# Optimization experiments

Hardware: AMD Instinct MI355X
Metric: run time of the kernel (lower is better)

The kernel has to match this reference:

```python
import jax, jax.numpy as jnp
import numpy as np

B, S, D, H, F, L = 16, 512, 512, 8, 2048, 3  # L layers: 1 in blocks_1 + 2 in blocks_2
DK = D // H
EPS = 1e-5

def setup_inputs():
    key = jax.random.key(0)
    ks = jax.random.split(key, 10)
    sc = 1.0 / np.sqrt(D)
    return dict(
        q_embed_data=jax.random.normal(ks[0], (B, S, D), jnp.float32),
        qa_embed_data=jax.random.normal(ks[1], (B, S, D), jnp.float32),
        Wk=jax.random.normal(ks[2], (L, D, D), jnp.float32) * sc,
        bk=jnp.zeros((L, D), jnp.float32),
        Wv=jax.random.normal(ks[3], (L, D, D), jnp.float32) * sc,
        bv=jnp.zeros((L, D), jnp.float32),
        Wo=jax.random.normal(ks[4], (L, D, D), jnp.float32) * sc,
        bo=jnp.zeros((L, D), jnp.float32),
        gammas=jax.random.normal(ks[5], (L, H, 1, 1), jnp.float32) * 0.5,
        ln1_g=jnp.ones((L, D), jnp.float32),
        ln1_b=jnp.zeros((L, D), jnp.float32),
        W1=jax.random.normal(ks[6], (L, D, F), jnp.float32) * sc,
        b1=jnp.zeros((L, F), jnp.float32),
        W2=jax.random.normal(ks[7], (L, F, D), jnp.float32) * (1.0 / np.sqrt(F)),
        b2=jnp.zeros((L, D), jnp.float32),
        ln2_g=jnp.ones((L, D), jnp.float32),
        ln2_b=jnp.zeros((L, D), jnp.float32),
    )

def _ln(x, g, b):
    m = jnp.mean(x, -1, keepdims=True)
    v = jnp.mean((x - m) ** 2, -1, keepdims=True)
    return (x - m) * jax.lax.rsqrt(v + EPS) * g + b

def _attention(q, k, v, mask, gamma):
    # q,k,v: [B,H,S,DK]; mask: [1,1,S,S] bool; gamma: [H,1,1]
    scores = jnp.einsum('bhid,bhjd->bhij', q, k) / np.sqrt(DK)
    maskf = mask.astype(scores.dtype)
    # first (no-grad in torch) softmax pass for distance decay
    p = jax.nn.softmax(jnp.where(mask, scores, -1e32), axis=-1) * maskf
    distcum = jnp.cumsum(p, axis=-1)
    disttot = jnp.sum(p, axis=-1, keepdims=True)
    idx = jnp.arange(scores.shape[-1])
    pos = jnp.abs(idx[None, :] - idx[:, None]).astype(scores.dtype)[None, None]
    dist = jax.lax.stop_gradient(
        jnp.sqrt(jnp.clip((disttot - distcum) * pos, 0.0, None)))
    g = -jax.nn.softplus(gamma)[None]  # [1,H,1,1]
    total_effect = jnp.clip(jnp.exp(dist * g), 1e-5, 1e5)
    scores = jnp.where(mask, scores * total_effect, -1e32)
    attn = jax.nn.softmax(scores, axis=-1)
    return jnp.einsum('bhij,bhjd->bhid', attn, v)

def _mha(q_in, k_in, v_in, mask, Wk, bk, Wv, bv, Wo, bo, gamma):
    bsz = q_in.shape[0]
    def proj(x, W, b):
        return (x @ W + b).reshape(bsz, -1, H, DK).transpose(0, 2, 1, 3)
    q = proj(q_in, Wk, bk)  # kq_same=True -> q uses k_linear
    k = proj(k_in, Wk, bk)
    v = proj(v_in, Wv, bv)
    o = _attention(q, k, v, mask, gamma)
    o = o.transpose(0, 2, 1, 3).reshape(bsz, -1, D)
    return o @ Wo + bo

def _block(i, mask, query, key, values, apply_pos, P):
    q2 = _mha(query, key, values, mask, P['Wk'][i], P['bk'][i], P['Wv'][i],
              P['bv'][i], P['Wo'][i], P['bo'][i], P['gammas'][i])
    x = _ln(query + q2, P['ln1_g'][i], P['ln1_b'][i])
    if apply_pos:
        h = jax.nn.relu(x @ P['W1'][i] + P['b1'][i]) @ P['W2'][i] + P['b2'][i]
        x = _ln(x + h, P['ln2_g'][i], P['ln2_b'][i])
    return x

def reference(q_embed_data, qa_embed_data, Wk, bk, Wv, bv, Wo, bo, gammas,
              ln1_g, ln1_b, W1, b1, W2, b2, ln2_g, ln2_b):
    P = dict(Wk=Wk, bk=bk, Wv=Wv, bv=bv, Wo=Wo, bo=bo, gammas=gammas,
             ln1_g=ln1_g, ln1_b=ln1_b, W1=W1, b1=b1, W2=W2, b2=b2,
             ln2_g=ln2_g, ln2_b=ln2_b)
    s = q_embed_data.shape[1]
    mask1 = jnp.tril(jnp.ones((s, s), bool))[None, None]        # mask==1: current+past
    mask0 = jnp.tril(jnp.ones((s, s), bool), -1)[None, None]    # mask==0: strictly past
    y = qa_embed_data
    x = q_embed_data
    y = _block(0, mask1, y, y, y, True, P)    # blocks_1: knowledge encoder
    x = _block(1, mask1, x, x, x, False, P)   # blocks_2: question encoder (no FFN)
    x = _block(2, mask0, x, x, y, True, P)    # blocks_2: knowledge retriever
    return x
```

## Files before the change

kernel.cpp:

```cpp
#include <hip/hip_runtime.h>
#include <hip/hip_bf16.h>

#define Bdim 16
#define Sdim 512
#define Ddim 512
#define Hdim 8
#define DKdim 64
#define Fdim 2048
#define Mrows (Bdim * Sdim)

typedef __attribute__((ext_vector_type(8))) short  frag16;
typedef __attribute__((ext_vector_type(4))) float  f32x4;
typedef __attribute__((ext_vector_type(8))) unsigned short ushort8;
typedef __attribute__((ext_vector_type(4))) unsigned short ushort4v;

#if defined(__has_builtin)
#  if __has_builtin(__builtin_amdgcn_exp2f)
#    define EXP2(x) __builtin_amdgcn_exp2f(x)
#  endif
#endif
#ifndef EXP2
#  define EXP2(x) __expf((x) * 0.6931471805599453f)
#endif
#define SC2 0.18033688011112042f

__device__ __forceinline__ unsigned short f2b(float x) {
    union { float f; unsigned int u; } v; v.f = x;
    unsigned int r = (v.u + 0x7FFFu + ((v.u >> 16) & 1u)) >> 16;
    return (unsigned short)r;
}

__global__ __launch_bounds__(256) void gemm_mfma(
    const __hip_bfloat16* __restrict__ A, const __hip_bfloat16* __restrict__ Bt,
    const float* __restrict__ bias, const float* __restrict__ R,
    float* __restrict__ Cf, unsigned short* __restrict__ Cb,
    int M, int N, int K, int do_relu)
{
    __shared__ short As[2][128 * 32];
    __shared__ short Bs[2][128 * 32];

    const int t = threadIdx.x;
    const int lane = t & 63;
    const int wave = t >> 6;

    const int gx = gridDim.x;
    const int nb = gx * gridDim.y;
    const int lid = blockIdx.x + gx * blockIdx.y;
    const int wid = (lid & 7) * (nb >> 3) + (lid >> 3);
    const int bm = (wid / gx) * 128;
    const int bn = (wid % gx) * 128;

    const int wm = (wave >> 1) * 64;
    const int wn = (wave & 1) * 64;

    f32x4 acc[4][4] = {};
    const int lrow = lane >> 2;
    const int lcol = (lane & 3) * 8;

    auto stage = [&](int k0, int buf) {
#pragma unroll
        for (int i = 0; i < 2; ++i) {
            const int chunk = wave * 2 + i;
            const int row = chunk * 16 + lrow;
            const __hip_bfloat16* ga = A + (size_t)(bm + row) * K + k0 + lcol;
            const __hip_bfloat16* gb = Bt + (size_t)(bn + row) * K + k0 + lcol;
            __builtin_amdgcn_global_load_lds(
                (const __attribute__((address_space(1))) unsigned int*)ga,
                (__attribute__((address_space(3))) unsigned int*)(&As[buf][chunk * 512]),
                16, 0, 0);
            __builtin_amdgcn_global_load_lds(
                (const __attribute__((address_space(1))) unsigned int*)gb,
                (__attribute__((address_space(3))) unsigned int*)(&Bs[buf][chunk * 512]),
                16, 0, 0);
        }
    };

    const int fr = lane & 15;
    const int quad = lane >> 4;
    const int nk = K >> 5;

    stage(0, 0);
    __syncthreads();

    for (int it = 0; it < nk; ++it) {
        const int buf = it & 1;
        if (it + 1 < nk) stage((it + 1) << 5, buf ^ 1);
        frag16 af[4], bfr[4];
#pragma unroll
        for (int i = 0; i < 4; ++i) {
            af[i]  = *(const frag16*)(&As[buf][(wm + i * 16 + fr) * 32 + quad * 8]);
            bfr[i] = *(const frag16*)(&Bs[buf][(wn + i * 16 + fr) * 32 + quad * 8]);
        }
#pragma unroll
        for (int mi = 0; mi < 4; ++mi)
#pragma unroll
            for (int ni = 0; ni < 4; ++ni)
                acc[mi][ni] = __builtin_amdgcn_mfma_f32_16x16x32_bf16(
                    af[mi], bfr[ni], acc[mi][ni], 0, 0, 0);
        __syncthreads();
    }

#pragma unroll
    for (int mi = 0; mi < 4; ++mi) {
#pragma unroll
        for (int r = 0; r < 4; ++r) {
            const int m = bm + wm + mi * 16 + quad * 4 + r;
#pragma unroll
            for (int ni = 0; ni < 4; ++ni) {
                const int n = bn + wn + ni * 16 + fr;
                float v = acc[mi][ni][r] + bias[n];
                if (R) v += R[(size_t)m * N + n];
                if (do_relu) v = fmaxf(v, 0.f);
                if (Cf) Cf[(size_t)m * N + n] = v;
                if (Cb) Cb[(size_t)m * N + n] = f2b(v);
            }
        }
    }
}

__global__ __launch_bounds__(256) void gemm_n64(
    const unsigned short* __restrict__ A0, const unsigned short* __restrict__ A1,
    const unsigned short* __restrict__ B0, const unsigned short* __restrict__ B1,
    const float* __restrict__ bias0, const float* __restrict__ bias1,
    const float* __restrict__ R, float* __restrict__ Cf,
    unsigned short* __restrict__ Cb, unsigned short* __restrict__ CbT,
    int K)
{
    const int NN = 512;
    __shared__ short As[2][128 * 64];
    __shared__ short Bs[2][64 * 64];

    const int trans = blockIdx.z;
    const unsigned short* A  = trans ? A1 : A0;
    const unsigned short* Bt = trans ? B1 : B0;
    const float* bias        = trans ? bias1 : bias0;

    const int t = threadIdx.x;
    const int lane = t & 63;
    const int wave = t >> 6;

    const int lid = blockIdx.x + 8 * blockIdx.y;
    const int wid = (lid & 7) * 64 + (lid >> 3);
    const int bm = (wid >> 3) * 128;
    const int bn = (wid & 7) * 64;

    const int wm = (wave >> 1) * 64;
    const int wn = (wave & 1) * 32;

    f32x4 acc[4][2] = {};

    const int srcslot = (((lane & 7) ^ (lane >> 3)) << 3);
    const int rsub = lane >> 3;

    auto stage = [&](int k0, int buf) {
#pragma unroll
        for (int i = 0; i < 4; ++i) {
            const int row = i * 32 + wave * 8 + rsub;
            const unsigned short* ga = A + (size_t)(bm + row) * K + k0 + srcslot;
            __builtin_amdgcn_global_load_lds(
                (const __attribute__((address_space(1))) unsigned int*)ga,
                (__attribute__((address_space(3))) unsigned int*)(&As[buf][(i * 256 + wave * 64) * 8]),
                16, 0, 0);
        }
#pragma unroll
        for (int i = 0; i < 2; ++i) {
            const int row = i * 32 + wave * 8 + rsub;
            const unsigned short* gb = Bt + (size_t)(bn + row) * K + k0 + srcslot;
            __builtin_amdgcn_global_load_lds(
                (const __attribute__((address_space(1))) unsigned int*)gb,
                (__attribute__((address_space(3))) unsigned int*)(&Bs[buf][(i * 256 + wave * 64) * 8]),
                16, 0, 0);
        }
    };

    const int fr = lane & 15;
    const int quad = lane >> 4;
    const int sw = (fr & 7) << 3;
    const int nk = K >> 6;

    stage(0, 0);
    __syncthreads();

    for (int it = 0; it < nk; ++it) {
        const int buf = it & 1;
        if (it + 1 < nk) stage((it + 1) << 6, buf ^ 1);
        frag16 af[2][4], bfr[2][2];
#pragma unroll
        for (int ks = 0; ks < 2; ++ks) {
            const int col = (ks * 32 + quad * 8) ^ sw;
#pragma unroll
            for (int i = 0; i < 4; ++i)
                af[ks][i] = *(const frag16*)(&As[buf][(wm + i * 16 + fr) * 64 + col]);
#pragma unroll
            for (int i = 0; i < 2; ++i)
                bfr[ks][i] = *(const frag16*)(&Bs[buf][(wn + i * 16 + fr) * 64 + col]);
        }
#pragma unroll
        for (int ks = 0; ks < 2; ++ks)
#pragma unroll
            for (int mi = 0; mi < 4; ++mi)
#pragma unroll
                for (int ni = 0; ni < 2; ++ni)
                    acc[mi][ni] = __builtin_amdgcn_mfma_f32_16x16x32_bf16(
                        af[ks][mi], bfr[ks][ni], acc[mi][ni], 0, 0, 0);
        __syncthreads();
    }

    if (trans) {
#pragma unroll
        for (int mi = 0; mi < 4; ++mi)
#pragma unroll
            for (int ni = 0; ni < 2; ++ni) {
                const int m = bm + wm + mi * 16 + quad * 4;
                const int n = bn + wn + ni * 16 + fr;
                ushort4v o;
#pragma unroll
                for (int r = 0; r < 4; ++r) o[r] = f2b(acc[mi][ni][r] + bias[n]);
                const int bb = m >> 9, s = m & 511;
                const int hh = n >> 6, dd = n & 63;
                *(ushort4v*)(CbT + (((size_t)((bb * Hdim + hh) * DKdim + dd)) << 9) + s) = o;
            }
        return;
    }

#pragma unroll
    for (int mi = 0; mi < 4; ++mi) {
#pragma unroll
        for (int r = 0; r < 4; ++r) {
            const int m = bm + wm + mi * 16 + quad * 4 + r;
#pragma unroll
            for (int ni = 0; ni < 2; ++ni) {
                const int n = bn + wn + ni * 16 + fr;
                float v = acc[mi][ni][r] + bias[n];
                if (R) v += R[(size_t)m * NN + n];
                if (Cf) Cf[(size_t)m * NN + n] = v;
                if (Cb) Cb[(size_t)m * NN + n] = f2b(v);
            }
        }
    }
}

__global__ __launch_bounds__(256) void gemm_kv4(
    const unsigned short* __restrict__ Ya, const unsigned short* __restrict__ Xa,
    const unsigned short* __restrict__ BtK0, const unsigned short* __restrict__ BtV0,
    const unsigned short* __restrict__ BtK1, const unsigned short* __restrict__ BtV1,
    const float* __restrict__ bk0, const float* __restrict__ bv0,
    const float* __restrict__ bk1, const float* __restrict__ bv1,
    unsigned short* __restrict__ K0, unsigned short* __restrict__ V0t,
    unsigned short* __restrict__ K1, unsigned short* __restrict__ V1t)
{
    const int K = 512;
    __shared__ short As[2][128 * 64];
    __shared__ short Bs[2][64 * 64];

    const int z = blockIdx.z;
    const unsigned short* A  = (z < 2) ? Ya : Xa;
    const unsigned short* Bt = (z == 0) ? BtK0 : (z == 1) ? BtV0 : (z == 2) ? BtK1 : BtV1;
    const float* bias        = (z == 0) ? bk0 : (z == 1) ? bv0 : (z == 2) ? bk1 : bv1;
    const int trans = z & 1;

    const int t = threadIdx.x;
    const int lane = t & 63;
    const int wave = t >> 6;

    const int lid = blockIdx.x + 8 * blockIdx.y;
    const int wid = (lid & 7) * 64 + (lid >> 3);
    const int bm = (wid >> 3) * 128;
    const int bn = (wid & 7) * 64;

    const int wm = (wave >> 1) * 64;
    const int wn = (wave & 1) * 32;

    f32x4 acc[4][2] = {};
    const int srcslot = (((lane & 7) ^ (lane >> 3)) << 3);
    const int rsub = lane >> 3;

    auto stage = [&](int k0, int buf) {
#pragma unroll
        for (int i = 0; i < 4; ++i) {
            const int row = i * 32 + wave * 8 + rsub;
            const unsigned short* ga = A + (size_t)(bm + row) * K + k0 + srcslot;
            __builtin_amdgcn_global_load_lds(
                (const __attribute__((address_space(1))) unsigned int*)ga,
                (__attribute__((address_space(3))) unsigned int*)(&As[buf][(i * 256 + wave * 64) * 8]),
                16, 0, 0);
        }
#pragma unroll
        for (int i = 0; i < 2; ++i) {
            const int row = i * 32 + wave * 8 + rsub;
            const unsigned short* gb = Bt + (size_t)(bn + row) * K + k0 + srcslot;
            __builtin_amdgcn_global_load_lds(
                (const __attribute__((address_space(1))) unsigned int*)gb,
                (__attribute__((address_space(3))) unsigned int*)(&Bs[buf][(i * 256 + wave * 64) * 8]),
                16, 0, 0);
        }
    };

    const int fr = lane & 15;
    const int quad = lane >> 4;
    const int sw = (fr & 7) << 3;
    const int nk = K >> 6;

    stage(0, 0);
    __syncthreads();

    for (int it = 0; it < nk; ++it) {
        const int buf = it & 1;
        if (it + 1 < nk) stage((it + 1) << 6, buf ^ 1);
        frag16 af[2][4], bfr[2][2];
#pragma unroll
        for (int ks = 0; ks < 2; ++ks) {
            const int col = (ks * 32 + quad * 8) ^ sw;
#pragma unroll
            for (int i = 0; i < 4; ++i)
                af[ks][i] = *(const frag16*)(&As[buf][(wm + i * 16 + fr) * 64 + col]);
#pragma unroll
            for (int i = 0; i < 2; ++i)
                bfr[ks][i] = *(const frag16*)(&Bs[buf][(wn + i * 16 + fr) * 64 + col]);
        }
#pragma unroll
        for (int ks = 0; ks < 2; ++ks)
#pragma unroll
            for (int mi = 0; mi < 4; ++mi)
#pragma unroll
                for (int ni = 0; ni < 2; ++ni)
                    acc[mi][ni] = __builtin_amdgcn_mfma_f32_16x16x32_bf16(
                        af[ks][mi], bfr[ks][ni], acc[mi][ni], 0, 0, 0);
        __syncthreads();
    }

    if (trans) {
        unsigned short* CbT = (z == 1) ? V0t : V1t;
#pragma unroll
        for (int mi = 0; mi < 4; ++mi)
#pragma unroll
            for (int ni = 0; ni < 2; ++ni) {
                const int m = bm + wm + mi * 16 + quad * 4;
                const int n = bn + wn + ni * 16 + fr;
                ushort4v o;
#pragma unroll
                for (int r = 0; r < 4; ++r) o[r] = f2b(acc[mi][ni][r] + bias[n]);
                const int bb = m >> 9, s = m & 511;
                const int hh = n >> 6, dd = n & 63;
                *(ushort4v*)(CbT + (((size_t)((bb * Hdim + hh) * DKdim + dd)) << 9) + s) = o;
            }
    } else {
        unsigned short* Cb = (z == 0) ? K0 : K1;
#pragma unroll
        for (int mi = 0; mi < 4; ++mi)
#pragma unroll
            for (int r = 0; r < 4; ++r) {
                const int m = bm + wm + mi * 16 + quad * 4 + r;
#pragma unroll
                for (int ni = 0; ni < 2; ++ni) {
                    const int n = bn + wn + ni * 16 + fr;
                    Cb[(size_t)m * 512 + n] = f2b(acc[mi][ni][r] + bias[n]);
                }
            }
    }
}

__global__ __launch_bounds__(256) void gemm_o2(
    const unsigned short* __restrict__ A0, const unsigned short* __restrict__ A1,
    const unsigned short* __restrict__ B0, const unsigned short* __restrict__ B1,
    const float* __restrict__ bias0, const float* __restrict__ bias1,
    const float* __restrict__ R0, const float* __restrict__ R1,
    float* __restrict__ C0, float* __restrict__ C1)
{
    const int K = 512;
    __shared__ short As[2][128 * 64];
    __shared__ short Bs[2][64 * 64];

    const int z = blockIdx.z;
    const unsigned short* A  = z ? A1 : A0;
    const unsigned short* Bt = z ? B1 : B0;
    const float* bias        = z ? bias1 : bias0;
    const float* R           = z ? R1 : R0;
    float* Cf                = z ? C1 : C0;

    const int t = threadIdx.x;
    const int lane = t & 63;
    const int wave = t >> 6;

    const int lid = blockIdx.x + 8 * blockIdx.y;
    const int wid = (lid & 7) * 64 + (lid >> 3);
    const int bm = (wid >> 3) * 128;
    const int bn = (wid & 7) * 64;

    const int wm = (wave >> 1) * 64;
    const int wn = (wave & 1) * 32;

    f32x4 acc[4][2] = {};
    const int srcslot = (((lane & 7) ^ (lane >> 3)) << 3);
    const int rsub = lane >> 3;

    auto stage = [&](int k0, int buf) {
#pragma unroll
        for (int i = 0; i < 4; ++i) {
            const int row = i * 32 + wave * 8 + rsub;
            const unsigned short* ga = A + (size_t)(bm + row) * K + k0 + srcslot;
            __builtin_amdgcn_global_load_lds(
                (const __attribute__((address_space(1))) unsigned int*)ga,
                (__attribute__((address_space(3))) unsigned int*)(&As[buf][(i * 256 + wave * 64) * 8]),
                16, 0, 0);
        }
#pragma unroll
        for (int i = 0; i < 2; ++i) {
            const int row = i * 32 + wave * 8 + rsub;
            const unsigned short* gb = Bt + (size_t)(bn + row) * K + k0 + srcslot;
            __builtin_amdgcn_global_load_lds(
                (const __attribute__((address_space(1))) unsigned int*)gb,
                (__attribute__((address_space(3))) unsigned int*)(&Bs[buf][(i * 256 + wave * 64) * 8]),
                16, 0, 0);
        }
    };

    const int fr = lane & 15;
    const int quad = lane >> 4;
    const int sw = (fr & 7) << 3;
    const int nk = K >> 6;

    stage(0, 0);
    __syncthreads();

    for (int it = 0; it < nk; ++it) {
        const int buf = it & 1;
        if (it + 1 < nk) stage((it + 1) << 6, buf ^ 1);
        frag16 af[2][4], bfr[2][2];
#pragma unroll
        for (int ks = 0; ks < 2; ++ks) {
            const int col = (ks * 32 + quad * 8) ^ sw;
#pragma unroll
            for (int i = 0; i < 4; ++i)
                af[ks][i] = *(const frag16*)(&As[buf][(wm + i * 16 + fr) * 64 + col]);
#pragma unroll
            for (int i = 0; i < 2; ++i)
                bfr[ks][i] = *(const frag16*)(&Bs[buf][(wn + i * 16 + fr) * 64 + col]);
        }
#pragma unroll
        for (int ks = 0; ks < 2; ++ks)
#pragma unroll
            for (int mi = 0; mi < 4; ++mi)
#pragma unroll
                for (int ni = 0; ni < 2; ++ni)
                    acc[mi][ni] = __builtin_amdgcn_mfma_f32_16x16x32_bf16(
                        af[ks][mi], bfr[ks][ni], acc[mi][ni], 0, 0, 0);
        __syncthreads();
    }

#pragma unroll
    for (int mi = 0; mi < 4; ++mi) {
#pragma unroll
        for (int r = 0; r < 4; ++r) {
            const int m = bm + wm + mi * 16 + quad * 4 + r;
#pragma unroll
            for (int ni = 0; ni < 2; ++ni) {
                const int n = bn + wn + ni * 16 + fr;
                Cf[(size_t)m * 512 + n] = acc[mi][ni][r] + bias[n] + R[(size_t)m * 512 + n];
            }
        }
    }
}

__global__ __launch_bounds__(256) void conv_b2(
    const float* __restrict__ X0, unsigned short* __restrict__ Y0,
    const float* __restrict__ X1, unsigned short* __restrict__ Y1,
    int halfBlocks)
{
    const int bid = blockIdx.x;
    const float* X = (bid < halfBlocks) ? X0 : X1;
    unsigned short* Y = (bid < halfBlocks) ? Y0 : Y1;
    const int lb = (bid < halfBlocks) ? bid : bid - halfBlocks;
    const size_t i = ((size_t)lb * 256 + threadIdx.x) * 8;
    float4 a = *(const float4*)(X + i);
    float4 b = *(const float4*)(X + i + 4);
    ushort8 o;
    o[0] = f2b(a.x); o[1] = f2b(a.y); o[2] = f2b(a.z); o[3] = f2b(a.w);
    o[4] = f2b(b.x); o[5] = f2b(b.y); o[6] = f2b(b.z); o[7] = f2b(b.w);
    *(ushort8*)(Y + i) = o;
}

__global__ __launch_bounds__(256) void wtrans_all(
    const float* __restrict__ Wk, const float* __restrict__ Wv,
    const float* __restrict__ Wo, const float* __restrict__ W1,
    const float* __restrict__ W2, unsigned short* __restrict__ dst)
{
    const int bid = blockIdx.x;
    const float* src; unsigned short* d; int K, N, tk, tn;
    if (bid < 576) {
        const int mat = bid >> 6, tile = bid & 63;
        const int l = mat / 3, wch = mat % 3;
        const float* W = (wch == 0) ? Wk : (wch == 1) ? Wv : Wo;
        src = W + (size_t)l * 262144;
        d = dst + (size_t)mat * 262144;
        K = 512; N = 512; tn = tile & 7; tk = tile >> 3;
    } else if (bid < 1088) {
        const int idx = bid - 576, l2 = idx >> 8, tile = idx & 255;
        src = W1 + (size_t)(l2 * 2) * (512 * 2048);
        d = dst + 9 * 262144 + (size_t)l2 * (512 * 2048);
        K = 512; N = 2048; tn = tile & 31; tk = tile >> 5;
    } else {
        const int idx = bid - 1088, l2 = idx >> 8, tile = idx & 255;
        src = W2 + (size_t)(l2 * 2) * (2048 * 512);
        d = dst + 9 * 262144 + 2 * (512 * 2048) + (size_t)l2 * (2048 * 512);
        K = 2048; N = 512; tn = tile & 7; tk = tile >> 3;
    }
    const int n0 = tn * 64, k0 = tk * 64;
    __shared__ float T[64][65];
    const int t = threadIdx.x;
    const int kl = t >> 4, n4 = (t & 15) << 2;
#pragma unroll
    for (int it = 0; it < 4; ++it) {
        const int k = kl + it * 16;
        float4 v = *(const float4*)(src + (size_t)(k0 + k) * N + n0 + n4);
        T[n4 + 0][k] = v.x; T[n4 + 1][k] = v.y;
        T[n4 + 2][k] = v.z; T[n4 + 3][k] = v.w;
    }
    __syncthreads();
    const int nl = t >> 3, k8 = (t & 7) << 3;
#pragma unroll
    for (int it = 0; it < 2; ++it) {
        const int n = nl + it * 32;
        ushort8 o;
#pragma unroll
        for (int c = 0; c < 8; ++c) o[c] = f2b(T[n][k8 + c]);
        *(ushort8*)(d + (size_t)(n0 + n) * K + k0 + k8) = o;
    }
}

__global__ __launch_bounds__(256, 8) void attn_flash8(
    const unsigned short* __restrict__ Kb0, const unsigned short* __restrict__ Vt0,
    const unsigned short* __restrict__ Kb1, const unsigned short* __restrict__ Vt1,
    const float* __restrict__ gam,
    unsigned short* __restrict__ Ob0, unsigned short* __restrict__ Ob1,
    int mask_type, int dual)
{
    __shared__ float CTw[16 * 33];
    __shared__ unsigned short Pst[4][16 * 36];
    __shared__ float S1s[4][16];
    __shared__ float S2s[4][16];
    __shared__ float OaccA[16 * 66];
    __shared__ float OaccB[16 * 66];

    int bh, layer;
    if (dual) { layer = blockIdx.x & 1; bh = blockIdx.x >> 1; }
    else      { layer = 0;              bh = blockIdx.x; }
    const unsigned short* Kb = layer ? Kb1 : Kb0;
    const unsigned short* Vt = layer ? Vt1 : Vt0;
    unsigned short* Ob       = layer ? Ob1 : Ob0;
    const float* g           = gam + layer * Hdim;

    const int h = bh & 7, b = bh >> 3;
    const int rk = blockIdx.y;
    const int tile = mask_type ? (31 - rk) : (rk == 0 ? 0 : 32 - rk);

    const int t = threadIdx.x, lane = t & 63, w = t >> 6;
    const int quad = lane >> 4, fr = lane & 15;
    const int q0 = tile * 16;
    const int iRow = q0 + fr;

    const unsigned short* kbase = Kb + (size_t)b * Sdim * Ddim + h * DKdim;
    const unsigned short* vtb = Vt + (size_t)(b * Hdim + h) * DKdim * Sdim;
    const float gneg2 = -log1pf(__expf(g[h])) * 1.4426950408889634f;

    frag16 aq0 = *(const frag16*)(kbase + (size_t)(q0 + fr) * Ddim + quad * 8);
    frag16 aq1 = *(const frag16*)(kbase + (size_t)(q0 + fr) * Ddim + 32 + quad * 8);

    float psum = 0.f;
    for (int jn = w; jn <= tile; jn += 4) {
        frag16 k0 = *(const frag16*)(kbase + (size_t)(jn * 16 + fr) * Ddim + quad * 8);
        frag16 k1 = *(const frag16*)(kbase + (size_t)(jn * 16 + fr) * Ddim + 32 + quad * 8);
        f32x4 z = {0.f, 0.f, 0.f, 0.f};
        z = __builtin_amdgcn_mfma_f32_16x16x32_bf16(k0, aq0, z, 0, 0, 0);
        z = __builtin_amdgcn_mfma_f32_16x16x32_bf16(k1, aq1, z, 0, 0, 0);
        float tq = 0.f;
        if (jn < tile) {
#pragma unroll
            for (int r = 0; r < 4; ++r) tq += EXP2(z[r] * SC2);
        } else {
#pragma unroll
            for (int r = 0; r < 4; ++r) {
                const bool valid = mask_type ? (quad * 4 + r <= fr)
                                             : (quad * 4 + r < fr);
                tq += valid ? EXP2(z[r] * SC2) : 0.f;
            }
        }
        psum += tq;
        float tt = tq;
        tt += __shfl_xor(tt, 16);
        tt += __shfl_xor(tt, 32);
        if (quad == 0) CTw[fr * 33 + jn] = tt;
    }
    {
        float s1 = psum;
        s1 += __shfl_xor(s1, 16);
        s1 += __shfl_xor(s1, 32);
        if (lane < 16) S1s[w][lane] = s1;
    }
    __syncthreads();

    if (w == 0 && lane < 16) {
        float run = 0.f;
        for (int jn = tile; jn >= 0; --jn) {
            const float tv = CTw[lane * 33 + jn];
            CTw[lane * 33 + jn] = run;
            run += tv;
        }
    }
    __syncthreads();

    const float rsum1 = 1.f / (S1s[0][fr] + S1s[1][fr] + S1s[2][fr] + S1s[3][fr]);
    unsigned short* Pw = Pst[w];
    const bool fm_blk = (mask_type == 0) && (tile == 0);
    const bool fmrow = fm_blk && (fr == 0);
    const int umax = fm_blk ? (Sdim / 32 - 1) : (tile >> 1);
    float sum2p = 0.f;
    f32x4 oacc[4] = {};

    for (int u = umax - w; u >= 0; u -= 4) {
#pragma unroll
        for (int half = 0; half < 2; ++half) {
            const int jn = 2 * u + half;
            uint2 pku;
            if (jn > tile) {
                const unsigned int pv = fmrow ? 0x3F803F80u : 0u;
                pku.x = pv; pku.y = pv;
                sum2p += fmrow ? 4.f : 0.f;
            } else {
                frag16 k0 = *(const frag16*)(kbase + (size_t)(jn * 16 + fr) * Ddim + quad * 8);
                frag16 k1 = *(const frag16*)(kbase + (size_t)(jn * 16 + fr) * Ddim + 32 + quad * 8);
                f32x4 z = {0.f, 0.f, 0.f, 0.f};
                z = __builtin_amdgcn_mfma_f32_16x16x32_bf16(k0, aq0, z, 0, 0, 0);
                z = __builtin_amdgcn_mfma_f32_16x16x32_bf16(k1, aq1, z, 0, 0, 0);
                const bool full = (jn < tile);
                float s2r[4], lsuf[4];
                float tq = 0.f;
#pragma unroll
                for (int r = 3; r >= 0; --r) {
                    lsuf[r] = tq;
                    s2r[r] = z[r] * SC2;
                    float e1 = EXP2(s2r[r]);
                    if (!full) {
                        const bool valid = mask_type ? (quad * 4 + r <= fr)
                                                     : (quad * 4 + r < fr);
                        e1 = valid ? e1 : 0.f;
                    }
                    tq += e1;
                }
                float incl = tq;
                {
                    float u1 = __shfl_down(incl, 16);
                    incl += (quad < 3) ? u1 : 0.f;
                    float u2 = __shfl_down(incl, 32);
                    incl += (quad < 2) ? u2 : 0.f;
                }
                const float base = CTw[fr * 33 + jn] + (incl - tq);
                const float pos0 = (float)(iRow - (jn * 16 + quad * 4));
                float e2v[4];
#pragma unroll
                for (int r = 0; r < 4; ++r) {
                    const float ratio = (base + lsuf[r]) * rsum1;
                    const float arg = ratio * fabsf(pos0 - (float)r);
                    const float te = fmaxf(EXP2(gneg2 * sqrtf(arg)), 1e-5f);
                    float e2 = EXP2(s2r[r] * te);
                    if (!full) {
                        const bool valid = mask_type ? (quad * 4 + r <= fr)
                                                     : (quad * 4 + r < fr);
                        e2 = valid ? e2 : (fmrow ? 1.f : 0.f);
                    }
                    sum2p += e2;
                    e2v[r] = e2;
                }
                union { __hip_bfloat162 hh; unsigned int u; } c0, c1;
                c0.hh = __float22bfloat162_rn(make_float2(e2v[0], e2v[1]));
                c1.hh = __float22bfloat162_rn(make_float2(e2v[2], e2v[3]));
                pku.x = c0.u; pku.y = c1.u;
            }
            *(uint2*)(Pw + fr * 36 + half * 16 + quad * 4) = pku;
        }
        frag16 pf = *(const frag16*)(Pw + fr * 36 + quad * 8);
        const int jb = u * 32;
#pragma unroll
        for (int dt = 0; dt < 4; ++dt) {
            frag16 vf = *(const frag16*)(vtb + (size_t)(dt * 16 + fr) * Sdim + jb + quad * 8);
            oacc[dt] = __builtin_amdgcn_mfma_f32_16x16x32_bf16(pf, vf, oacc[dt], 0, 0, 0);
        }
    }

    {
        float s2 = sum2p;
        s2 += __shfl_xor(s2, 16);
        s2 += __shfl_xor(s2, 32);
        if (lane < 16) S2s[w][lane] = s2;
    }
    if (w == 1) {
#pragma unroll
        for (int dt = 0; dt < 4; ++dt)
#pragma unroll
            for (int r = 0; r < 4; ++r)
                OaccA[(quad * 4 + r) * 66 + dt * 16 + fr] = oacc[dt][r];
    }
    if (w == 3) {
#pragma unroll
        for (int dt = 0; dt < 4; ++dt)
#pragma unroll
            for (int r = 0; r < 4; ++r)
                OaccB[(quad * 4 + r) * 66 + dt * 16 + fr] = oacc[dt][r];
    }
    __syncthreads();
    if (w == 0) {
#pragma unroll
        for (int dt = 0; dt < 4; ++dt)
#pragma unroll
            for (int r = 0; r < 4; ++r)
                oacc[dt][r] += OaccA[(quad * 4 + r) * 66 + dt * 16 + fr];
    }
    if (w == 2) {
#pragma unroll
        for (int dt = 0; dt < 4; ++dt)
#pragma unroll
            for (int r = 0; r < 4; ++r)
                oacc[dt][r] += OaccB[(quad * 4 + r) * 66 + dt * 16 + fr];
    }
    __syncthreads();
    if (w == 2) {
#pragma unroll
        for (int dt = 0; dt < 4; ++dt)
#pragma unroll
            for (int r = 0; r < 4; ++r)
                OaccA[(quad * 4 + r) * 66 + dt * 16 + fr] = oacc[dt][r];
    }
    __syncthreads();

    if (w == 0) {
        const float rs2 = 1.f / (S2s[0][fr] + S2s[1][fr] + S2s[2][fr] + S2s[3][fr]);
        float rs2q[4];
#pragma unroll
        for (int r = 0; r < 4; ++r) rs2q[r] = __shfl(rs2, quad * 4 + r);

        unsigned short* obase = Ob + ((size_t)(b * Sdim + q0)) * Ddim + h * DKdim;
#pragma unroll
        for (int dt = 0; dt < 4; ++dt)
#pragma unroll
            for (int r = 0; r < 4; ++r) {
                const float v = oacc[dt][r] + OaccA[(quad * 4 + r) * 66 + dt * 16 + fr];
                obase[(size_t)(quad * 4 + r) * Ddim + dt * 16 + fr] = f2b(v * rs2q[r]);
            }
    }
}

__device__ __forceinline__ void ln_row(
    const float* __restrict__ X, const float* __restrict__ g,
    const float* __restrict__ bta, float* __restrict__ Y,
    unsigned short* __restrict__ Yb, int row, int t,
    float* r1, float* r2)
{
    const float* x = X + (size_t)row * Ddim;
    float a = x[t], b = x[t + 256];
    r1[t] = a + b;
    r2[t] = a * a + b * b;
    __syncthreads();
    for (int off = 128; off; off >>= 1) {
        if (t < off) { r1[t] += r1[t + off]; r2[t] += r2[t + off]; }
        __syncthreads();
    }
    float mean = r1[0] * (1.f / Ddim);
    float var = r2[0] * (1.f / Ddim) - mean * mean;
    float rs = rsqrtf(var + 1e-5f);
    float y0 = (a - mean) * rs * g[t] + bta[t];
    float y1 = (b - mean) * rs * g[t + 256] + bta[t + 256];
    if (Y) {
        float* y = Y + (size_t)row * Ddim;
        y[t] = y0;
        y[t + 256] = y1;
    }
    if (Yb) {
        unsigned short* yb = Yb + (size_t)row * Ddim;
        yb[t] = f2b(y0);
        yb[t + 256] = f2b(y1);
    }
}

__global__ __launch_bounds__(256) void ln_kernel(
    const float* __restrict__ X, const float* __restrict__ g,
    const float* __restrict__ bta, float* __restrict__ Y,
    unsigned short* __restrict__ Yb)
{
    __shared__ float r1[256], r2[256];
    ln_row(X, g, bta, Y, Yb, blockIdx.x, threadIdx.x, r1, r2);
}

__global__ __launch_bounds__(256) void ln_kernel2(
    const float* __restrict__ Xa, const float* __restrict__ ga,
    const float* __restrict__ ba, float* __restrict__ Ya,
    unsigned short* __restrict__ Yba,
    const float* __restrict__ Xb, const float* __restrict__ gb,
    const float* __restrict__ bb, float* __restrict__ Yb2,
    unsigned short* __restrict__ Ybb)
{
    __shared__ float r1[256], r2[256];
    const int row = blockIdx.x;
    if (row < Mrows)
        ln_row(Xa, ga, ba, Ya, Yba, row, threadIdx.x, r1, r2);
    else
        ln_row(Xb, gb, bb, Yb2, Ybb, row - Mrows, threadIdx.x, r1, r2);
}

extern "C" void kernel_launch(void* const* d_in, const int* in_sizes, int n_in,
                              void* d_out, int out_size, void* d_ws, size_t ws_size,
                              hipStream_t stream)
{
    const float* x0     = (const float*)d_in[0];
    const float* y0     = (const float*)d_in[1];
    const float* Wk     = (const float*)d_in[2];
    const float* bk     = (const float*)d_in[3];
    const float* Wv     = (const float*)d_in[4];
    const float* bv     = (const float*)d_in[5];
    const float* Wo     = (const float*)d_in[6];
    const float* bo     = (const float*)d_in[7];
    const float* gammas = (const float*)d_in[8];
    const float* ln1g   = (const float*)d_in[9];
    const float* ln1b   = (const float*)d_in[10];
    const float* W1     = (const float*)d_in[11];
    const float* b1     = (const float*)d_in[12];
    const float* W2     = (const float*)d_in[13];
    const float* b2     = (const float*)d_in[14];
    const float* ln2g   = (const float*)d_in[15];
    const float* ln2b   = (const float*)d_in[16];

    const size_t NBSD = (size_t)Mrows * Ddim;
    float* ws = (float*)d_ws;
    float* T1   = ws;
    float* X1   = T1 + NBSD;
    float* Xbuf = X1 + NBSD;
    unsigned short* Kbf = (unsigned short*)(Xbuf + NBSD);
    unsigned short* Vt  = Kbf + NBSD;
    unsigned short* AOb = Vt + NBSD;
    unsigned short* Abf = AOb + NBSD;
    unsigned short* Xbf = Abf + NBSD;
    unsigned short* Ybf = Xbf + NBSD;
    unsigned short* Hbb = Ybf + NBSD;
    unsigned short* WtAll = Hbb + (size_t)Mrows * Fdim;

    unsigned short* Xb_in = Hbb;
    unsigned short* AOb1  = Hbb + NBSD;
    unsigned short* Yb_in = Hbb + 2 * NBSD;
    unsigned short* Kbf1  = Abf;
    unsigned short* Vt1   = Ybf;
    float* T1b = (float*)d_out;

    auto WtK = [&](int l) { return WtAll + (size_t)(l * 3 + 0) * 262144; };
    auto WtV = [&](int l) { return WtAll + (size_t)(l * 3 + 1) * 262144; };
    auto WtO = [&](int l) { return WtAll + (size_t)(l * 3 + 2) * 262144; };
    auto Wt1 = [&](int l) { return WtAll + 9 * 262144 + (size_t)(l >> 1) * (512 * 2048); };
    auto Wt2 = [&](int l) { return WtAll + 9 * 262144 + 2 * (512 * 2048) + (size_t)(l >> 1) * (2048 * 512); };

    const int convBlocks = (int)(NBSD / 2048);

    wtrans_all<<<1600, 256, 0, stream>>>(Wk, Wv, Wo, W1, W2, WtAll);
    conv_b2<<<2 * convBlocks, 256, 0, stream>>>(y0, Yb_in, x0, Xb_in, convBlocks);
    gemm_kv4<<<dim3(8, 64, 4), 256, 0, stream>>>(
        Yb_in, Xb_in, WtK(0), WtV(0), WtK(1), WtV(1),
        bk, bv, bk + Ddim, bv + Ddim,
        Kbf, Vt, Kbf1, Vt1);
    attn_flash8<<<dim3(2 * Bdim * Hdim, Sdim / 16, 1), 256, 0, stream>>>(
        Kbf, Vt, Kbf1, Vt1, gammas, AOb, AOb1, 1, 1);
    gemm_o2<<<dim3(8, 64, 2), 256, 0, stream>>>(
        AOb, AOb1, WtO(0), WtO(1), bo, bo + Ddim, y0, x0, T1, T1b);
    ln_kernel2<<<2 * Mrows, 256, 0, stream>>>(
        T1, ln1g, ln1b, X1, Abf,
        T1b, ln1g + Ddim, ln1b + Ddim, Xbuf, Xbf);
    gemm_mfma<<<dim3(Fdim / 128, Mrows / 128), 256, 0, stream>>>(
        (const __hip_bfloat16*)Abf, (const __hip_bfloat16*)Wt1(0),
        b1, nullptr, nullptr, Hbb, Mrows, Fdim, Ddim, 1);
    gemm_n64<<<dim3(8, 64, 1), 256, 0, stream>>>(
        Hbb, Hbb, Wt2(0), Wt2(0), b2, b2,
        X1, T1, nullptr, nullptr, Fdim);
    ln_kernel<<<Mrows, 256, 0, stream>>>(T1, ln2g, ln2b, nullptr, Ybf);

    const int l = 2;
    gemm_n64<<<dim3(8, 64, 2), 256, 0, stream>>>(
        Xbf, Ybf, WtK(l), WtV(l), bk + l * Ddim, bv + l * Ddim,
        nullptr, nullptr, Kbf, Vt, Ddim);
    attn_flash8<<<dim3(Bdim * Hdim, Sdim / 16, 1), 256, 0, stream>>>(
        Kbf, Vt, Kbf, Vt, gammas + (size_t)l * Hdim, AOb, AOb, 0, 0);
    gemm_n64<<<dim3(8, 64, 1), 256, 0, stream>>>(
        AOb, AOb, WtO(l), WtO(l), bo + l * Ddim, bo + l * Ddim,
        Xbuf, T1, nullptr, nullptr, Ddim);
    ln_kernel<<<Mrows, 256, 0, stream>>>(T1,
        ln1g + (size_t)l * Ddim, ln1b + (size_t)l * Ddim, X1, Abf);
    gemm_mfma<<<dim3(Fdim / 128, Mrows / 128), 256, 0, stream>>>(
        (const __hip_bfloat16*)Abf, (const __hip_bfloat16*)Wt1(l),
        b1 + (size_t)l * Fdim, nullptr, nullptr, Hbb, Mrows, Fdim, Ddim, 1);
    gemm_n64<<<dim3(8, 64, 1), 256, 0, stream>>>(
        Hbb, Hbb, Wt2(l), Wt2(l), b2 + (size_t)l * Ddim, b2 + (size_t)l * Ddim,
        X1, T1, nullptr, nullptr, Fdim);
    ln_kernel<<<Mrows, 256, 0, stream>>>(T1,
        ln2g + (size_t)l * Ddim, ln2b + (size_t)l * Ddim, (float*)d_out, nullptr);
}
```

Measured before the change: 575.3 us.

## Split-K the FFN down-projection and fold partial sums into wave-per-row LayerNorm

The FFN second GEMM (K=2048) becomes a two-way split-K kernel. One K-half writes bias plus residual plus its partial sum, and the other writes a raw partial into a float buffer that aliases the AOb/Abf scratch space. The following LayerNorm adds the two partials. LayerNorm is also rewritten to use one wave per row with float4 loads and shuffle reductions, replacing the 256-thread shared-memory tree with its many barriers. The aim is more blocks for the down-projection and cheaper normalisation, at the cost of extra partial-buffer traffic and a reliance on the scratch aliasing being safe.

```diff
diff --git a/kernel.cpp b/kernel.cpp
--- a/kernel.cpp
+++ b/kernel.cpp
@@ -235,6 +235,105 @@
                 if (R) v += R[(size_t)m * NN + n];
                 if (Cf) Cf[(size_t)m * NN + n] = v;
                 if (Cb) Cb[(size_t)m * NN + n] = f2b(v);
+            }
+        }
+    }
+}
+
+__global__ __launch_bounds__(256) void gemm_ffn2(
+    const unsigned short* __restrict__ A, const unsigned short* __restrict__ Bt,
+    const float* __restrict__ bias, const float* __restrict__ R,
+    float* __restrict__ C0, float* __restrict__ C1)
+{
+    const int K = 2048, KH = 1024;
+    __shared__ short As[2][128 * 64];
+    __shared__ short Bs[2][64 * 64];
+
+    const int z = blockIdx.z;
+    const int kbase = z * KH;
+
+    const int t = threadIdx.x;
+    const int lane = t & 63;
+    const int wave = t >> 6;
+
+    const int lid = blockIdx.x + 8 * blockIdx.y;
+    const int wid = (lid & 7) * 64 + (lid >> 3);
+    const int bm = (wid >> 3) * 128;
+    const int bn = (wid & 7) * 64;
+
+    const int wm = (wave >> 1) * 64;
+    const int wn = (wave & 1) * 32;
+
+    f32x4 acc[4][2] = {};
+    const int srcslot = (((lane & 7) ^ (lane >> 3)) << 3);
+    const int rsub = lane >> 3;
+
+    auto stage = [&](int k0, int buf) {
+#pragma unroll
+        for (int i = 0; i < 4; ++i) {
+            const int row = i * 32 + wave * 8 + rsub;
+            const unsigned short* ga = A + (size_t)(bm + row) * K + k0 + srcslot;
+            __builtin_amdgcn_global_load_lds(
+                (const __attribute__((address_space(1))) unsigned int*)ga,
+                (__attribute__((address_space(3))) unsigned int*)(&As[buf][(i * 256 + wave * 64) * 8]),
+                16, 0, 0);
+        }
+#pragma unroll
+        for (int i = 0; i < 2; ++i) {
+            const int row = i * 32 + wave * 8 + rsub;
+            const unsigned short* gb = Bt + (size_t)(bn + row) * K + k0 + srcslot;
+            __builtin_amdgcn_global_load_lds(
+                (const __attribute__((address_space(1))) unsigned int*)gb,
+                (__attribute__((address_space(3))) unsigned int*)(&Bs[buf][(i * 256 + wave * 64) * 8]),
+                16, 0, 0);
+        }
+    };
+
+    const int fr = lane & 15;
+    const int quad = lane >> 4;
+    const int sw = (fr & 7) << 3;
+    const int nk = KH >> 6;
+
+    stage(kbase, 0);
+    __syncthreads();
+
+    for (int it = 0; it < nk; ++it) {
+        const int buf = it & 1;
+        if (it + 1 < nk) stage(kbase + ((it + 1) << 6), buf ^ 1);
+        frag16 af[2][4], bfr[2][2];
+#pragma unroll
+        for (int ks = 0; ks < 2; ++ks) {
+            const int col = (ks * 32 + quad * 8) ^ sw;
+#pragma unroll
+            for (int i = 0; i < 4; ++i)
+                af[ks][i] = *(const frag16*)(&As[buf][(wm + i * 16 + fr) * 64 + col]);
+#pragma unroll
+            for (int i = 0; i < 2; ++i)
+                bfr[ks][i] = *(const frag16*)(&Bs[buf][(wn + i * 16 + fr) * 64 + col]);
+        }
+#pragma unroll
+        for (int ks = 0; ks < 2; ++ks)
+#pragma unroll
+            for (int mi = 0; mi < 4; ++mi)
+#pragma unroll
+                for (int ni = 0; ni < 2; ++ni)
+                    acc[mi][ni] = __builtin_amdgcn_mfma_f32_16x16x32_bf16(
+                        af[ks][mi], bfr[ks][ni], acc[mi][ni], 0, 0, 0);
+        __syncthreads();
+    }
+
+#pragma unroll
+    for (int mi = 0; mi < 4; ++mi) {
+#pragma unroll
+        for (int r = 0; r < 4; ++r) {
+            const int m = bm + wm + mi * 16 + quad * 4 + r;
+#pragma unroll
+            for (int ni = 0; ni < 2; ++ni) {
+                const int n = bn + wn + ni * 16 + fr;
+                if (z == 0)
+                    C0[(size_t)m * 512 + n] = acc[mi][ni][r] + bias[n] + R[(size_t)m * 512 + n];
+                else
+                    C1[(size_t)m * 512 + n] = acc[mi][ni][r];
             }
         }
     }
@@ -749,48 +848,67 @@
     }
 }
 
-__device__ __forceinline__ void ln_row(
-    const float* __restrict__ X, const float* __restrict__ g,
-    const float* __restrict__ bta, float* __restrict__ Y,
-    unsigned short* __restrict__ Yb, int row, int t,
-    float* r1, float* r2)
-{
-    const float* x = X + (size_t)row * Ddim;
-    float a = x[t], b = x[t + 256];
-    r1[t] = a + b;
-    r2[t] = a * a + b * b;
-    __syncthreads();
-    for (int off = 128; off; off >>= 1) {
-        if (t < off) { r1[t] += r1[t + off]; r2[t] += r2[t + off]; }
-        __syncthreads();
-    }
-    float mean = r1[0] * (1.f / Ddim);
-    float var = r2[0] * (1.f / Ddim) - mean * mean;
-    float rs = rsqrtf(var + 1e-5f);
-    float y0 = (a - mean) * rs * g[t] + bta[t];
-    float y1 = (b - mean) * rs * g[t + 256] + bta[t + 256];
+__device__ __forceinline__ void ln_row_wave(
+    const float* __restrict__ X, const float* __restrict__ P,
+    const float* __restrict__ g, const float* __restrict__ bta,
+    float* __restrict__ Y, unsigned short* __restrict__ Yb,
+    int row, int lane)
+{
+    const size_t base = (size_t)row * Ddim + lane * 8;
+    float4 a = *(const float4*)(X + base);
+    float4 b = *(const float4*)(X + base + 4);
+    if (P) {
+        float4 pa = *(const float4*)(P + base);
+        float4 pb = *(const float4*)(P + base + 4);
+        a.x += pa.x; a.y += pa.y; a.z += pa.z; a.w += pa.w;
+        b.x += pb.x; b.y += pb.y; b.z += pb.z; b.w += pb.w;
+    }
+    float s  = a.x + a.y + a.z + a.w + b.x + b.y + b.z + b.w;
+    float s2 = a.x * a.x + a.y * a.y + a.z * a.z + a.w * a.w
+             + b.x * b.x + b.y * b.y + b.z * b.z + b.w * b.w;
+#pragma unroll
+    for (int off = 1; off < 64; off <<= 1) {
+        s  += __shfl_xor(s, off);
+        s2 += __shfl_xor(s2, off);
+    }
+    const float mean = s * (1.f / Ddim);
+    const float var = s2 * (1.f / Ddim) - mean * mean;
+    const float rs = rsqrtf(var + 1e-5f);
+    float4 ga = *(const float4*)(g + lane * 8);
+    float4 gb = *(const float4*)(g + lane * 8 + 4);
+    float4 ba = *(const float4*)(bta + lane * 8);
+    float4 bb = *(const float4*)(bta + lane * 8 + 4);
+    float y[8];
+    y[0] = (a.x - mean) * rs * ga.x + ba.x;
+    y[1] = (a.y - mean) * rs * ga.y + ba.y;
+    y[2] = (a.z - mean) * rs * ga.z + ba.z;
+    y[3] = (a.w - mean) * rs * ga.w + ba.w;
+    y[4] = (b.x - mean) * rs * gb.x + bb.x;
+    y[5] = (b.y - mean) * rs * gb.y + bb.y;
+    y[6] = (b.z - mean) * rs * gb.z + bb.z;
+    y[7] = (b.w - mean) * rs * gb.w + bb.w;
     if (Y) {
-        float* y = Y + (size_t)row * Ddim;
-        y[t] = y0;
-        y[t + 256] = y1;
+        *(float4*)(Y + base)     = make_float4(y[0], y[1], y[2], y[3]);
+        *(float4*)(Y + base + 4) = make_float4(y[4], y[5], y[6], y[7]);
     }
     if (Yb) {
-        unsigned short* yb = Yb + (size_t)row * Ddim;
-        yb[t] = f2b(y0);
-        yb[t + 256] = f2b(y1);
-    }
-}
-
-__global__ __launch_bounds__(256) void ln_kernel(
-    const float* __restrict__ X, const float* __restrict__ g,
-    const float* __restrict__ bta, float* __restrict__ Y,
-    unsigned short* __restrict__ Yb)
-{
-    __shared__ float r1[256], r2[256];
-    ln_row(X, g, bta, Y, Yb, blockIdx.x, threadIdx.x, r1, r2);
-}
-
-__global__ __launch_bounds__(256) void ln_kernel2(
+        ushort8 o;
+#pragma unroll
+        for (int c = 0; c < 8; ++c) o[c] = f2b(y[c]);
+        *(ushort8*)(Yb + base) = o;
+    }
+}
+
+__global__ __launch_bounds__(256) void ln_w1(
+    const float* __restrict__ X, const float* __restrict__ P,
+    const float* __restrict__ g, const float* __restrict__ bta,
+    float* __restrict__ Y, unsigned short* __restrict__ Yb)
+{
+    const int row = blockIdx.x * 4 + (threadIdx.x >> 6);
+    ln_row_wave(X, P, g, bta, Y, Yb, row, threadIdx.x & 63);
+}
+
+__global__ __launch_bounds__(256) void ln_w2(
     const float* __restrict__ Xa, const float* __restrict__ ga,
     const float* __restrict__ ba, float* __restrict__ Ya,
     unsigned short* __restrict__ Yba,
@@ -798,12 +916,11 @@
     const float* __restrict__ bb, float* __restrict__ Yb2,
     unsigned short* __restrict__ Ybb)
 {
-    __shared__ float r1[256], r2[256];
-    const int row = blockIdx.x;
+    const int row = blockIdx.x * 4 + (threadIdx.x >> 6);
     if (row < Mrows)
-        ln_row(Xa, ga, ba, Ya, Yba, row, threadIdx.x, r1, r2);
+        ln_row_wave(Xa, nullptr, ga, ba, Ya, Yba, row, threadIdx.x & 63);
     else
-        ln_row(Xb, gb, bb, Yb2, Ybb, row - Mrows, threadIdx.x, r1, r2);
+        ln_row_wave(Xb, nullptr, gb, bb, Yb2, Ybb, row - Mrows, threadIdx.x & 63);
 }
 
 extern "C" void kernel_launch(void* const* d_in, const int* in_sizes, int n_in,
@@ -848,6 +965,7 @@
     unsigned short* Kbf1  = Abf;
     unsigned short* Vt1   = Ybf;
     float* T1b = (float*)d_out;
+    float* P1  = (float*)AOb;
 
     auto WtK = [&](int l) { return WtAll + (size_t)(l * 3 + 0) * 262144; };
     auto WtV = [&](int l) { return WtAll + (size_t)(l * 3 + 1) * 262144; };
@@ -867,16 +985,15 @@
         Kbf, Vt, Kbf1, Vt1, gammas, AOb, AOb1, 1, 1);
     gemm_o2<<<dim3(8, 64, 2), 256, 0, stream>>>(
         AOb, AOb1, WtO(0), WtO(1), bo, bo + Ddim, y0, x0, T1, T1b);
-    ln_kernel2<<<2 * Mrows, 256, 0, stream>>>(
+    ln_w2<<<2 * Mrows / 4, 256, 0, stream>>>(
         T1, ln1g, ln1b, X1, Abf,
         T1b, ln1g + Ddim, ln1b + Ddim, Xbuf, Xbf);
     gemm_mfma<<<dim3(Fdim / 128, Mrows / 128), 256, 0, stream>>>(
         (const __hip_bfloat16*)Abf, (const __hip_bfloat16*)Wt1(0),
         b1, nullptr, nullptr, Hbb, Mrows, Fdim, Ddim, 1);
-    gemm_n64<<<dim3(8, 64, 1), 256, 0, stream>>>(
-        Hbb, Hbb, Wt2(0), Wt2(0), b2, b2,
-        X1, T1, nullptr, nullptr, Fdim);
-    ln_kernel<<<Mrows, 256, 0, stream>>>(T1, ln2g, ln2b, nullptr, Ybf);
+    gemm_ffn2<<<dim3(8, 64, 2), 256, 0, stream>>>(
+        Hbb, Wt2(0), b2, X1, T1, P1);
+    ln_w1<<<Mrows / 4, 256, 0, stream>>>(T1, P1, ln2g, ln2b, nullptr, Ybf);
 
     const int l = 2;
     gemm_n64<<<dim3(8, 64, 2), 256, 0, stream>>>(
@@ -887,14 +1004,13 @@
     gemm_n64<<<dim3(8, 64, 1), 256, 0, stream>>>(
         AOb, AOb, WtO(l), WtO(l), bo + l * Ddim, bo + l * Ddim,
         Xbuf, T1, nullptr, nullptr, Ddim);
-    ln_kernel<<<Mrows, 256, 0, stream>>>(T1,
+    ln_w1<<<Mrows / 4, 256, 0, stream>>>(T1, nullptr,
         ln1g + (size_t)l * Ddim, ln1b + (size_t)l * Ddim, X1, Abf);
     gemm_mfma<<<dim3(Fdim / 128, Mrows / 128), 256, 0, stream>>>(
         (const __hip_bfloat16*)Abf, (const __hip_bfloat16*)Wt1(l),
         b1 + (size_t)l * Fdim, nullptr, nullptr, Hbb, Mrows, Fdim, Ddim, 1);
-    gemm_n64<<<dim3(8, 64, 1), 256, 0, stream>>>(
-        Hbb, Hbb, Wt2(l), Wt2(l), b2 + (size_t)l * Ddim, b2 + (size_t)l * Ddim,
-        X1, T1, nullptr, nullptr, Fdim);
-    ln_kernel<<<Mrows, 256, 0, stream>>>(T1,
+    gemm_ffn2<<<dim3(8, 64, 2), 256, 0, stream>>>(
+        Hbb, Wt2(l), b2 + (size_t)l * Ddim, X1, T1, P1);
+    ln_w1<<<Mrows / 4, 256, 0, stream>>>(T1, P1,
         ln2g + (size_t)l * Ddim, ln2b + (size_t)l * Ddim, (float*)d_out, nullptr);
 }
```

After: 562.4 us. -2.3%, faster.
